# Kernel tuning notes

Hardware: AMD Instinct MI355X
Metric: run time of the kernel (lower is better)

## Reference

```python
import jax, jax.numpy as jnp
import numpy as np

N, F, NEWF = 8192, 128, 64
NEG_INF = -1e10
LEAKY_ALPHA = 0.2


def setup_inputs() -> dict:
    key = jax.random.key(0)
    k1, k2, k3, k4, k5 = jax.random.split(key, 5)
    X = jax.random.normal(k1, (N, F), dtype=jnp.float32)
    A = jax.random.randint(k2, (N, N), 0, 2, dtype=jnp.int32)
    W = jax.random.normal(k3, (F, NEWF), dtype=jnp.float32) * (1.0 / np.sqrt(F))
    a_self = jax.random.normal(k4, (NEWF, 1), dtype=jnp.float32) * (1.0 / np.sqrt(NEWF))
    a_neigh = jax.random.normal(k5, (NEWF, 1), dtype=jnp.float32) * (1.0 / np.sqrt(NEWF))
    return {"X": X, "A": A, "W": W, "a_self": a_self, "a_neigh": a_neigh}


def reference(X, A, W, a_self, a_neigh):
    # Linear transform: [N, newF]
    h = X @ W
    # Additive attention logits: self_attn[i] + neigh_attn[j] -> [N, N]
    self_attn = h @ a_self      # [N, 1]
    neigh_attn = h @ a_neigh    # [N, 1]
    dense = self_attn + neigh_attn.T               # [N, N]
    dense = jax.nn.leaky_relu(dense, LEAKY_ALPHA)
    # Mask: -1e10 where A == 0, else 0
    masked = jnp.where(A == 0, dense + NEG_INF, dense)
    attn = jax.nn.softmax(masked, axis=-1)
    # Dropout is identity at inference (Keras Dropout without training=True)
    out = attn @ h                                  # [N, newF]
    return jax.nn.relu(out)
```

## Files before the change

kernel.cpp:

```cpp
#include <hip/hip_runtime.h>

#define N 8192
#define F 128
#define NEWF 64
#define ALPHA 0.2f
#define JSPLIT 8
#define JW (N / JSPLIT)
#define NCH (JW / 32)
#define RB 64

typedef float f32x4 __attribute__((ext_vector_type(4)));
typedef short short8 __attribute__((ext_vector_type(8)));

__global__ void k_hsn(const float* __restrict__ X, const float* __restrict__ W,
                      const float* __restrict__ a_self, const float* __restrict__ a_neigh,
                      float* __restrict__ h, float* __restrict__ s, float* __restrict__ n) {
    int row = blockIdx.x * 4 + (threadIdx.x >> 6);
    int l = threadIdx.x & 63;
    const float* xr = X + (size_t)row * F;
    float acc = 0.0f;
#pragma unroll 8
    for (int f = 0; f < F; ++f) acc += xr[f] * W[f * NEWF + l];
    h[(size_t)row * NEWF + l] = acc;
    float ts = acc * a_self[l];
    float tn = acc * a_neigh[l];
#pragma unroll
    for (int off = 32; off; off >>= 1) {
        ts += __shfl_xor(ts, off);
        tn += __shfl_xor(tn, off);
    }
    if (l == 0) { s[row] = ts; n[row] = tn; }
}

__global__ void k_tr(const float* __restrict__ h, unsigned short* __restrict__ hThi,
                     unsigned short* __restrict__ hTlo) {
    __shared__ float tile[64][65];
    const int t = threadIdx.x;
    const int j0 = blockIdx.x * 64;
    {
        const int jr = t >> 2, cs = (t & 3) * 16;
        const float4* src = (const float4*)(h + (size_t)(j0 + jr) * NEWF + cs);
#pragma unroll
        for (int q = 0; q < 4; ++q) {
            float4 v = src[q];
            tile[jr][cs + q * 4 + 0] = v.x; tile[jr][cs + q * 4 + 1] = v.y;
            tile[jr][cs + q * 4 + 2] = v.z; tile[jr][cs + q * 4 + 3] = v.w;
        }
    }
    __syncthreads();
    {
        const int c = t >> 2, js = (t & 3) * 16;
        short8 hi0 = {}, hi1 = {}, lo0 = {}, lo1 = {};
#pragma unroll
        for (int k = 0; k < 16; ++k) {
            float v = tile[js + k][c];
            unsigned xb = __float_as_uint(v);
            short hb = (short)(xb >> 16);
            float lof = v - __uint_as_float(xb & 0xffff0000u);
            short lb = (short)(__float_as_uint(lof) >> 16);
            if (k < 8) { hi0[k] = hb; lo0[k] = lb; }
            else       { hi1[k - 8] = hb; lo1[k - 8] = lb; }
        }
        size_t off = (size_t)c * N + j0 + js;
        *(short8*)(hThi + off)     = hi0;
        *(short8*)(hThi + off + 8) = hi1;
        *(short8*)(hTlo + off)     = lo0;
        *(short8*)(hTlo + off + 8) = lo1;
    }
}

__global__ void k_nmax(const float* __restrict__ n, float* __restrict__ nmax) {
    __shared__ float red[1024];
    int t = threadIdx.x;
    float4 v0 = ((const float4*)n)[t];
    float4 v1 = ((const float4*)n)[t + 1024];
    float m = fmaxf(fmaxf(fmaxf(v0.x, v0.y), fmaxf(v0.z, v0.w)),
                    fmaxf(fmaxf(v1.x, v1.y), fmaxf(v1.z, v1.w)));
    red[t] = m;
    __syncthreads();
    for (int off = 512; off; off >>= 1) {
        if (t < off) red[t] = fmaxf(red[t], red[t + off]);
        __syncthreads();
    }
    if (t == 0) nmax[0] = red[0];
}

__global__ void __launch_bounds__(256, 4) k_main(
        const int* __restrict__ A, const float* __restrict__ s,
        const float* __restrict__ n, const float* __restrict__ nmaxp,
        const unsigned short* __restrict__ hThi, const unsigned short* __restrict__ hTlo,
        float* __restrict__ pacc, float* __restrict__ pz) {
    __shared__ __align__(16) unsigned short bt[2][2][64][32];

    const int tid = threadIdx.x;
    const int w = tid >> 6, l = tid & 63;
    const int lr = l & 15, lg = l >> 4;

    const int rb = blockIdx.x / JSPLIT;
    const int js = blockIdx.x % JSPLIT;
    const int r0 = rb * RB + w * 16;
    const int jb = js * JW;

    const float sval = s[r0 + lr];
    const float tM = sval + nmaxp[0];
    const float Mv = fmaxf(tM, ALPHA * tM);
    float zacc = 0.0f;

    f32x4 acc0 = {0.f,0.f,0.f,0.f}, acc1 = {0.f,0.f,0.f,0.f};
    f32x4 acc2 = {0.f,0.f,0.f,0.f}, acc3 = {0.f,0.f,0.f,0.f};

    const int srow = tid >> 2, sj = (tid & 3) * 8;
    const short8* ghi = (const short8*)(hThi + (size_t)srow * N + jb + sj);
    const short8* glo = (const short8*)(hTlo + (size_t)srow * N + jb + sj);

    {
        short8 vhi = ghi[0];
        short8 vlo = glo[0];
        *(short8*)&bt[0][0][srow][sj] = vhi;
        *(short8*)&bt[0][1][srow][sj] = vlo;
    }
    asm volatile("s_waitcnt lgkmcnt(0)" ::: "memory");
    __builtin_amdgcn_s_barrier();

    const int4*   Ap  = (const int4*)(A + (size_t)(r0 + lr) * N + jb + lg * 8);
    const float4* npv = (const float4*)(n + jb + lg * 8);

    int4 a0 = Ap[0], a1 = Ap[1];
    float4 nv0 = npv[0], nv1 = npv[1];

    for (int c = 0; c < NCH; ++c) {
        const int p = c & 1;
        const int cn = (c + 1 < NCH) ? c + 1 : 0;

        short8 nhi = ghi[cn * 4];
        short8 nlo = glo[cn * 4];
        int4   na0 = Ap[cn * 8], na1 = Ap[cn * 8 + 1];
        float4 nn0 = npv[cn * 8], nn1 = npv[cn * 8 + 1];
        __builtin_amdgcn_sched_barrier(0);

        int   av[8] = {a0.x, a0.y, a0.z, a0.w, a1.x, a1.y, a1.z, a1.w};
        float nf[8] = {nv0.x, nv0.y, nv0.z, nv0.w, nv1.x, nv1.y, nv1.z, nv1.w};
        short8 ahi, alo;
#pragma unroll
        for (int j = 0; j < 8; ++j) {
            float t  = sval + nf[j];
            float lv = fmaxf(t, ALPHA * t);
            float ex = __expf(lv - Mv);
            ex = (av[j] != 0) ? ex : 0.0f;
            zacc += ex;
            unsigned xb = __float_as_uint(ex);
            ahi[j] = (short)(xb >> 16);
            float lof = ex - __uint_as_float(xb & 0xffff0000u);
            alo[j] = (short)(__float_as_uint(lof) >> 16);
        }

        short8 B0h = *(const short8*)&bt[p][0][lr +  0][lg * 8];
        short8 B1h = *(const short8*)&bt[p][0][lr + 16][lg * 8];
        short8 B2h = *(const short8*)&bt[p][0][lr + 32][lg * 8];
        short8 B3h = *(const short8*)&bt[p][0][lr + 48][lg * 8];
        short8 B0l = *(const short8*)&bt[p][1][lr +  0][lg * 8];
        short8 B1l = *(const short8*)&bt[p][1][lr + 16][lg * 8];
        short8 B2l = *(const short8*)&bt[p][1][lr + 32][lg * 8];
        short8 B3l = *(const short8*)&bt[p][1][lr + 48][lg * 8];

        acc0 = __builtin_amdgcn_mfma_f32_16x16x32_bf16(ahi, B0h, acc0, 0, 0, 0);
        acc1 = __builtin_amdgcn_mfma_f32_16x16x32_bf16(ahi, B1h, acc1, 0, 0, 0);
        acc2 = __builtin_amdgcn_mfma_f32_16x16x32_bf16(ahi, B2h, acc2, 0, 0, 0);
        acc3 = __builtin_amdgcn_mfma_f32_16x16x32_bf16(ahi, B3h, acc3, 0, 0, 0);
        acc0 = __builtin_amdgcn_mfma_f32_16x16x32_bf16(ahi, B0l, acc0, 0, 0, 0);
        acc1 = __builtin_amdgcn_mfma_f32_16x16x32_bf16(ahi, B1l, acc1, 0, 0, 0);
        acc2 = __builtin_amdgcn_mfma_f32_16x16x32_bf16(ahi, B2l, acc2, 0, 0, 0);
        acc3 = __builtin_amdgcn_mfma_f32_16x16x32_bf16(ahi, B3l, acc3, 0, 0, 0);
        acc0 = __builtin_amdgcn_mfma_f32_16x16x32_bf16(alo, B0h, acc0, 0, 0, 0);
        acc1 = __builtin_amdgcn_mfma_f32_16x16x32_bf16(alo, B1h, acc1, 0, 0, 0);
        acc2 = __builtin_amdgcn_mfma_f32_16x16x32_bf16(alo, B2h, acc2, 0, 0, 0);
        acc3 = __builtin_amdgcn_mfma_f32_16x16x32_bf16(alo, B3h, acc3, 0, 0, 0);

        *(short8*)&bt[p ^ 1][0][srow][sj] = nhi;
        *(short8*)&bt[p ^ 1][1][srow][sj] = nlo;
        asm volatile("s_waitcnt lgkmcnt(0)" ::: "memory");
        __builtin_amdgcn_s_barrier();
        __builtin_amdgcn_sched_barrier(0);

        a0 = na0; a1 = na1; nv0 = nn0; nv1 = nn1;
    }

    zacc += __shfl_xor(zacc, 16);
    zacc += __shfl_xor(zacc, 32);

    float* pa = pacc + ((size_t)js * N + r0) * NEWF;
#pragma unroll
    for (int r = 0; r < 4; ++r) {
        int row = lg * 4 + r;
        pa[(size_t)row * NEWF +  0 + lr] = acc0[r];
        pa[(size_t)row * NEWF + 16 + lr] = acc1[r];
        pa[(size_t)row * NEWF + 32 + lr] = acc2[r];
        pa[(size_t)row * NEWF + 48 + lr] = acc3[r];
    }
    if (l < 16) pz[(size_t)js * N + r0 + lr] = zacc;
}

__global__ void k_fin(const float* __restrict__ pacc, const float* __restrict__ pz,
                      float* __restrict__ out) {
    int t = blockIdx.x * 256 + threadIdx.x;
    int i = t >> 6, k = t & 63;
    float v = 0.0f, z = 0.0f;
#pragma unroll
    for (int psl = 0; psl < JSPLIT; ++psl) {
        v += pacc[((size_t)psl * N + i) * NEWF + k];
        z += pz[(size_t)psl * N + i];
    }
    out[t] = fmaxf(v / z, 0.0f);
}

extern "C" void kernel_launch(void* const* d_in, const int* in_sizes, int n_in,
                              void* d_out, int out_size, void* d_ws, size_t ws_size,
                              hipStream_t stream) {
    const float* X       = (const float*)d_in[0];
    const int*   A       = (const int*)d_in[1];
    const float* W       = (const float*)d_in[2];
    const float* a_self  = (const float*)d_in[3];
    const float* a_neigh = (const float*)d_in[4];
    float* out = (float*)d_out;

    float* wsf = (float*)d_ws;
    float* h    = wsf;
    float* s    = h + (size_t)N * NEWF;
    float* nv   = s + N;
    float* nmax = nv + N;
    unsigned short* hThi = (unsigned short*)(nmax + 4);
    unsigned short* hTlo = hThi + (size_t)N * NEWF;
    float* pacc = (float*)(hTlo + (size_t)N * NEWF);
    float* pz   = pacc + (size_t)JSPLIT * N * NEWF;

    k_hsn <<<N / 4,        256, 0, stream>>>(X, W, a_self, a_neigh, h, s, nv);
    k_tr  <<<N / 64,       256, 0, stream>>>(h, hThi, hTlo);
    k_nmax<<<1,           1024, 0, stream>>>(nv, nmax);
    k_main<<<(N / RB) * JSPLIT, 256, 0, stream>>>(A, s, nv, nmax, hThi, hTlo, pacc, pz);
    k_fin <<<(N * NEWF) / 256, 256, 0, stream>>>(pacc, pz, out);
}
```

Before: 432.1 us.

## Pack adjacency matrix into bitmask before main attention kernel

Adds a pre-pass kernel that reads the int32 adjacency matrix once and packs it into per-lane 32-bit bitmask words, laid out to match the main kernel's row/column-split access pattern. The main kernel then reads one mask word per four chunks instead of two int4 loads per chunk, which removes A-matrix bandwidth from the compute-heavy loop. The full 256MB A read still happens in the pack kernel, so the gain depends on that kernel being purely bandwidth-bound while the main kernel was latency or issue limited. It also adds an extra launch and a small workspace region.

```diff
diff --git a/kernel.cpp b/kernel.cpp
--- a/kernel.cpp
+++ b/kernel.cpp
@@ -11,6 +11,36 @@
 
 typedef float f32x4 __attribute__((ext_vector_type(4)));
 typedef short short8 __attribute__((ext_vector_type(8)));
+
+__global__ void __launch_bounds__(256) k_pack(const int* __restrict__ A,
+                                              unsigned* __restrict__ mask) {
+    const int t = threadIdx.x;
+    const int row = blockIdx.x * 8 + (t >> 5);
+    const int u = t & 31;
+    const int js = u >> 2, lg = u & 3;
+    const int4* src = (const int4*)(A + (size_t)row * N + js * JW + lg * 8);
+    unsigned* dst = mask + (((size_t)row * JSPLIT + js) * 4 + lg) * 8;
+#pragma unroll 4
+    for (int c4 = 0; c4 < 8; ++c4) {
+        unsigned word = 0;
+#pragma unroll
+        for (int k = 0; k < 4; ++k) {
+            const int4* p = src + (size_t)(c4 * 4 + k) * 8;
+            int4 a0 = p[0], a1 = p[1];
+            unsigned b = 0;
+            b |= (a0.x != 0) ? 1u   : 0u;
+            b |= (a0.y != 0) ? 2u   : 0u;
+            b |= (a0.z != 0) ? 4u   : 0u;
+            b |= (a0.w != 0) ? 8u   : 0u;
+            b |= (a1.x != 0) ? 16u  : 0u;
+            b |= (a1.y != 0) ? 32u  : 0u;
+            b |= (a1.z != 0) ? 64u  : 0u;
+            b |= (a1.w != 0) ? 128u : 0u;
+            word |= b << (8 * k);
+        }
+        dst[c4] = word;
+    }
+}
 
 __global__ void k_hsn(const float* __restrict__ X, const float* __restrict__ W,
                       const float* __restrict__ a_self, const float* __restrict__ a_neigh,
@@ -86,7 +116,7 @@
 }
 
 __global__ void __launch_bounds__(256, 4) k_main(
-        const int* __restrict__ A, const float* __restrict__ s,
+        const unsigned* __restrict__ mask, const float* __restrict__ s,
         const float* __restrict__ n, const float* __restrict__ nmaxp,
         const unsigned short* __restrict__ hThi, const unsigned short* __restrict__ hTlo,
         float* __restrict__ pacc, float* __restrict__ pz) {
@@ -112,6 +142,9 @@
     const int srow = tid >> 2, sj = (tid & 3) * 8;
     const short8* ghi = (const short8*)(hThi + (size_t)srow * N + jb + sj);
     const short8* glo = (const short8*)(hTlo + (size_t)srow * N + jb + sj);
+
+    const unsigned* mp = mask + (((size_t)(r0 + lr) * JSPLIT + js) * 4 + lg) * 8;
+    unsigned mpref = mp[0];
 
     {
         short8 vhi = ghi[0];
@@ -122,23 +155,25 @@
     asm volatile("s_waitcnt lgkmcnt(0)" ::: "memory");
     __builtin_amdgcn_s_barrier();
 
-    const int4*   Ap  = (const int4*)(A + (size_t)(r0 + lr) * N + jb + lg * 8);
     const float4* npv = (const float4*)(n + jb + lg * 8);
-
-    int4 a0 = Ap[0], a1 = Ap[1];
     float4 nv0 = npv[0], nv1 = npv[1];
+    unsigned mword = 0;
 
     for (int c = 0; c < NCH; ++c) {
         const int p = c & 1;
         const int cn = (c + 1 < NCH) ? c + 1 : 0;
 
+        if ((c & 3) == 0) {
+            mword = mpref;
+            mpref = mp[((c >> 2) + 1) & 7];
+        }
+        const unsigned mbyte = (mword >> ((c & 3) * 8)) & 0xffu;
+
         short8 nhi = ghi[cn * 4];
         short8 nlo = glo[cn * 4];
-        int4   na0 = Ap[cn * 8], na1 = Ap[cn * 8 + 1];
         float4 nn0 = npv[cn * 8], nn1 = npv[cn * 8 + 1];
         __builtin_amdgcn_sched_barrier(0);
 
-        int   av[8] = {a0.x, a0.y, a0.z, a0.w, a1.x, a1.y, a1.z, a1.w};
         float nf[8] = {nv0.x, nv0.y, nv0.z, nv0.w, nv1.x, nv1.y, nv1.z, nv1.w};
         short8 ahi, alo;
 #pragma unroll
@@ -146,7 +181,7 @@
             float t  = sval + nf[j];
             float lv = fmaxf(t, ALPHA * t);
             float ex = __expf(lv - Mv);
-            ex = (av[j] != 0) ? ex : 0.0f;
+            ex = (mbyte & (1u << j)) ? ex : 0.0f;
             zacc += ex;
             unsigned xb = __float_as_uint(ex);
             ahi[j] = (short)(xb >> 16);
@@ -182,7 +217,7 @@
         __builtin_amdgcn_s_barrier();
         __builtin_amdgcn_sched_barrier(0);
 
-        a0 = na0; a1 = na1; nv0 = nn0; nv1 = nn1;
+        nv0 = nn0; nv1 = nn1;
     }
 
     zacc += __shfl_xor(zacc, 16);
@@ -232,10 +267,12 @@
     unsigned short* hTlo = hThi + (size_t)N * NEWF;
     float* pacc = (float*)(hTlo + (size_t)N * NEWF);
     float* pz   = pacc + (size_t)JSPLIT * N * NEWF;
-
+    unsigned* mask = (unsigned*)(pz + (size_t)JSPLIT * N);
+
+    k_pack<<<N / 8,        256, 0, stream>>>(A, mask);
     k_hsn <<<N / 4,        256, 0, stream>>>(X, W, a_self, a_neigh, h, s, nv);
     k_tr  <<<N / 64,       256, 0, stream>>>(h, hThi, hTlo);
     k_nmax<<<1,           1024, 0, stream>>>(nv, nmax);
-    k_main<<<(N / RB) * JSPLIT, 256, 0, stream>>>(A, s, nv, nmax, hThi, hTlo, pacc, pz);
+    k_main<<<(N / RB) * JSPLIT, 256, 0, stream>>>(mask, s, nv, nmax, hThi, hTlo, pacc, pz);
     k_fin <<<(N * NEWF) / 256, 256, 0, stream>>>(pacc, pz, out);
 }
```

New measurement: 449.6 us. 4.1% more time.

## Stage hT tiles via direct global-to-LDS loads in larger swizzled pieces

Applied to the files above, without the earlier changes.

Replaces the per-32-column register-staged double buffer of hT hi/lo with global_load_lds DMA of 128-column pieces into a 32KB XOR-swizzled LDS slab. This cuts barriers to two per 4 chunks and avoids the VGPR round trip for B staging. In exchange, each piece load is no longer overlapped with compute (single buffer, wait vmcnt(0) before use), and the larger LDS footprint may lower occupancy.

```diff
diff --git a/kernel.cpp b/kernel.cpp
--- a/kernel.cpp
+++ b/kernel.cpp
@@ -6,11 +6,18 @@
 #define ALPHA 0.2f
 #define JSPLIT 8
 #define JW (N / JSPLIT)
-#define NCH (JW / 32)
 #define RB 64
+#define PIECE 128
+#define NPIECE (JW / PIECE)
 
 typedef float f32x4 __attribute__((ext_vector_type(4)));
 typedef short short8 __attribute__((ext_vector_type(8)));
+
+typedef const __attribute__((address_space(1))) unsigned* gp_t;
+typedef __attribute__((address_space(3))) unsigned* lp_t;
+static __device__ __forceinline__ void gload_lds16(const void* g, void* l) {
+    __builtin_amdgcn_global_load_lds((gp_t)g, (lp_t)l, 16, 0, 0);
+}
 
 __global__ void k_hsn(const float* __restrict__ X, const float* __restrict__ W,
                       const float* __restrict__ a_self, const float* __restrict__ a_neigh,
@@ -90,7 +97,7 @@
         const float* __restrict__ n, const float* __restrict__ nmaxp,
         const unsigned short* __restrict__ hThi, const unsigned short* __restrict__ hTlo,
         float* __restrict__ pacc, float* __restrict__ pz) {
-    __shared__ __align__(16) unsigned short bt[2][2][64][32];
+    __shared__ __align__(16) unsigned short slab[16384];
 
     const int tid = threadIdx.x;
     const int w = tid >> 6, l = tid & 63;
@@ -109,81 +116,96 @@
     f32x4 acc0 = {0.f,0.f,0.f,0.f}, acc1 = {0.f,0.f,0.f,0.f};
     f32x4 acc2 = {0.f,0.f,0.f,0.f}, acc3 = {0.f,0.f,0.f,0.f};
 
-    const int srow = tid >> 2, sj = (tid & 3) * 8;
-    const short8* ghi = (const short8*)(hThi + (size_t)srow * N + jb + sj);
-    const short8* glo = (const short8*)(hTlo + (size_t)srow * N + jb + sj);
-
-    {
-        short8 vhi = ghi[0];
-        short8 vlo = glo[0];
-        *(short8*)&bt[0][0][srow][sj] = vhi;
-        *(short8*)&bt[0][1][srow][sj] = vlo;
-    }
-    asm volatile("s_waitcnt lgkmcnt(0)" ::: "memory");
-    __builtin_amdgcn_s_barrier();
+    const int sr_lo = tid >> 4;
+    const int s_jsh = (((tid & 15) * 16) ^ ((sr_lo & 7) << 4)) >> 1;
+    char* slabc = (char*)slab;
+    const int rswz = (lr & 7) << 4;
+
+#define STAGE(piece)                                                          \
+    {                                                                         \
+        const size_t gcol = (size_t)jb + (size_t)(piece) * PIECE + s_jsh;     \
+        _Pragma("unroll")                                                     \
+        for (int q = 0; q < 8; ++q) {                                         \
+            const int r_ = (q & 3) * 16 + sr_lo;                              \
+            const unsigned short* gp_ =                                       \
+                ((q >> 2) ? hTlo : hThi) + (size_t)r_ * N + gcol;             \
+            gload_lds16(gp_, slabc + q * 4096 + tid * 16);                    \
+        }                                                                     \
+    }
 
     const int4*   Ap  = (const int4*)(A + (size_t)(r0 + lr) * N + jb + lg * 8);
     const float4* npv = (const float4*)(n + jb + lg * 8);
 
+    STAGE(0);
     int4 a0 = Ap[0], a1 = Ap[1];
     float4 nv0 = npv[0], nv1 = npv[1];
-
-    for (int c = 0; c < NCH; ++c) {
-        const int p = c & 1;
-        const int cn = (c + 1 < NCH) ? c + 1 : 0;
-
-        short8 nhi = ghi[cn * 4];
-        short8 nlo = glo[cn * 4];
-        int4   na0 = Ap[cn * 8], na1 = Ap[cn * 8 + 1];
-        float4 nn0 = npv[cn * 8], nn1 = npv[cn * 8 + 1];
-        __builtin_amdgcn_sched_barrier(0);
-
-        int   av[8] = {a0.x, a0.y, a0.z, a0.w, a1.x, a1.y, a1.z, a1.w};
-        float nf[8] = {nv0.x, nv0.y, nv0.z, nv0.w, nv1.x, nv1.y, nv1.z, nv1.w};
-        short8 ahi, alo;
-#pragma unroll
-        for (int j = 0; j < 8; ++j) {
-            float t  = sval + nf[j];
-            float lv = fmaxf(t, ALPHA * t);
-            float ex = __expf(lv - Mv);
-            ex = (av[j] != 0) ? ex : 0.0f;
-            zacc += ex;
-            unsigned xb = __float_as_uint(ex);
-            ahi[j] = (short)(xb >> 16);
-            float lof = ex - __uint_as_float(xb & 0xffff0000u);
-            alo[j] = (short)(__float_as_uint(lof) >> 16);
-        }
-
-        short8 B0h = *(const short8*)&bt[p][0][lr +  0][lg * 8];
-        short8 B1h = *(const short8*)&bt[p][0][lr + 16][lg * 8];
-        short8 B2h = *(const short8*)&bt[p][0][lr + 32][lg * 8];
-        short8 B3h = *(const short8*)&bt[p][0][lr + 48][lg * 8];
-        short8 B0l = *(const short8*)&bt[p][1][lr +  0][lg * 8];
-        short8 B1l = *(const short8*)&bt[p][1][lr + 16][lg * 8];
-        short8 B2l = *(const short8*)&bt[p][1][lr + 32][lg * 8];
-        short8 B3l = *(const short8*)&bt[p][1][lr + 48][lg * 8];
-
-        acc0 = __builtin_amdgcn_mfma_f32_16x16x32_bf16(ahi, B0h, acc0, 0, 0, 0);
-        acc1 = __builtin_amdgcn_mfma_f32_16x16x32_bf16(ahi, B1h, acc1, 0, 0, 0);
-        acc2 = __builtin_amdgcn_mfma_f32_16x16x32_bf16(ahi, B2h, acc2, 0, 0, 0);
-        acc3 = __builtin_amdgcn_mfma_f32_16x16x32_bf16(ahi, B3h, acc3, 0, 0, 0);
-        acc0 = __builtin_amdgcn_mfma_f32_16x16x32_bf16(ahi, B0l, acc0, 0, 0, 0);
-        acc1 = __builtin_amdgcn_mfma_f32_16x16x32_bf16(ahi, B1l, acc1, 0, 0, 0);
-        acc2 = __builtin_amdgcn_mfma_f32_16x16x32_bf16(ahi, B2l, acc2, 0, 0, 0);
-        acc3 = __builtin_amdgcn_mfma_f32_16x16x32_bf16(ahi, B3l, acc3, 0, 0, 0);
-        acc0 = __builtin_amdgcn_mfma_f32_16x16x32_bf16(alo, B0h, acc0, 0, 0, 0);
-        acc1 = __builtin_amdgcn_mfma_f32_16x16x32_bf16(alo, B1h, acc1, 0, 0, 0);
-        acc2 = __builtin_amdgcn_mfma_f32_16x16x32_bf16(alo, B2h, acc2, 0, 0, 0);
-        acc3 = __builtin_amdgcn_mfma_f32_16x16x32_bf16(alo, B3h, acc3, 0, 0, 0);
-
-        *(short8*)&bt[p ^ 1][0][srow][sj] = nhi;
-        *(short8*)&bt[p ^ 1][1][srow][sj] = nlo;
-        asm volatile("s_waitcnt lgkmcnt(0)" ::: "memory");
-        __builtin_amdgcn_s_barrier();
-        __builtin_amdgcn_sched_barrier(0);
-
-        a0 = na0; a1 = na1; nv0 = nn0; nv1 = nn1;
-    }
+    asm volatile("s_waitcnt vmcnt(0)" ::: "memory");
+    __builtin_amdgcn_s_barrier();
+    __builtin_amdgcn_sched_barrier(0);
+
+    for (int piece = 0; piece < NPIECE; ++piece) {
+#pragma unroll
+        for (int k = 0; k < 4; ++k) {
+            const int ci = piece * 4 + k;
+            const int cn = (ci + 1 < NPIECE * 4) ? ci + 1 : 0;
+
+            int4 na0 = Ap[(size_t)cn * 8], na1 = Ap[(size_t)cn * 8 + 1];
+            float4 nn0 = npv[(size_t)cn * 8], nn1 = npv[(size_t)cn * 8 + 1];
+            __builtin_amdgcn_sched_barrier(0);
+
+            int   av[8] = {a0.x, a0.y, a0.z, a0.w, a1.x, a1.y, a1.z, a1.w};
+            float nf[8] = {nv0.x, nv0.y, nv0.z, nv0.w, nv1.x, nv1.y, nv1.z, nv1.w};
+            short8 ahi, alo;
+#pragma unroll
+            for (int j = 0; j < 8; ++j) {
+                float t  = sval + nf[j];
+                float lv = fmaxf(t, ALPHA * t);
+                float ex = __expf(lv - Mv);
+                ex = (av[j] != 0) ? ex : 0.0f;
+                zacc += ex;
+                unsigned xb = __float_as_uint(ex);
+                ahi[j] = (short)(xb >> 16);
+                float lof = ex - __uint_as_float(xb & 0xffff0000u);
+                alo[j] = (short)(__float_as_uint(lof) >> 16);
+            }
+
+            const int joff = (k * 64 + lg * 16) ^ rswz;
+            const char* rp = (const char*)slab + lr * 256 + joff;
+            short8 B0h = *(const short8*)(rp);
+            short8 B1h = *(const short8*)(rp + 16 * 256);
+            short8 B2h = *(const short8*)(rp + 32 * 256);
+            short8 B3h = *(const short8*)(rp + 48 * 256);
+            short8 B0l = *(const short8*)(rp + 16384);
+            short8 B1l = *(const short8*)(rp + 16384 + 16 * 256);
+            short8 B2l = *(const short8*)(rp + 16384 + 32 * 256);
+            short8 B3l = *(const short8*)(rp + 16384 + 48 * 256);
+
+            acc0 = __builtin_amdgcn_mfma_f32_16x16x32_bf16(ahi, B0h, acc0, 0, 0, 0);
+            acc1 = __builtin_amdgcn_mfma_f32_16x16x32_bf16(ahi, B1h, acc1, 0, 0, 0);
+            acc2 = __builtin_amdgcn_mfma_f32_16x16x32_bf16(ahi, B2h, acc2, 0, 0, 0);
+            acc3 = __builtin_amdgcn_mfma_f32_16x16x32_bf16(ahi, B3h, acc3, 0, 0, 0);
+            acc0 = __builtin_amdgcn_mfma_f32_16x16x32_bf16(ahi, B0l, acc0, 0, 0, 0);
+            acc1 = __builtin_amdgcn_mfma_f32_16x16x32_bf16(ahi, B1l, acc1, 0, 0, 0);
+            acc2 = __builtin_amdgcn_mfma_f32_16x16x32_bf16(ahi, B2l, acc2, 0, 0, 0);
+            acc3 = __builtin_amdgcn_mfma_f32_16x16x32_bf16(ahi, B3l, acc3, 0, 0, 0);
+            acc0 = __builtin_amdgcn_mfma_f32_16x16x32_bf16(alo, B0h, acc0, 0, 0, 0);
+            acc1 = __builtin_amdgcn_mfma_f32_16x16x32_bf16(alo, B1h, acc1, 0, 0, 0);
+            acc2 = __builtin_amdgcn_mfma_f32_16x16x32_bf16(alo, B2h, acc2, 0, 0, 0);
+            acc3 = __builtin_amdgcn_mfma_f32_16x16x32_bf16(alo, B3h, acc3, 0, 0, 0);
+
+            a0 = na0; a1 = na1; nv0 = nn0; nv1 = nn1;
+        }
+
+        if (piece + 1 < NPIECE) {
+            __builtin_amdgcn_s_barrier();
+            __builtin_amdgcn_sched_barrier(0);
+            STAGE(piece + 1);
+            asm volatile("s_waitcnt vmcnt(0)" ::: "memory");
+            __builtin_amdgcn_s_barrier();
+            __builtin_amdgcn_sched_barrier(0);
+        }
+    }
+#undef STAGE
 
     zacc += __shfl_xor(zacc, 16);
     zacc += __shfl_xor(zacc, 32);
```

Measured after the change: 425.1 us. Within noise of the previous version (-1.6%).
